# Optimization experiments

Measured on AMD Instinct MI355X. Metric: run time of the kernel, lower is better.

## Reference

```python
import jax, jax.numpy as jnp
import numpy as np

N = 100000
E = 6400000
IN_CH = 128
HID = 8
HEADS = 2
OUT_CH = 1
NEG_SLOPE = 0.2


def gat_conv(x, src, dst, W, a_src, a_dst, bias, heads, out_ch, concat, n_nodes):
    # x: [N, F_in], W: [F_in, heads*out_ch], a_src/a_dst: [heads, out_ch]
    h = (x @ W).reshape(n_nodes, heads, out_ch)          # [N, H, C]
    alpha_s = jnp.sum(h * a_src[None], axis=-1)          # [N, H]
    alpha_d = jnp.sum(h * a_dst[None], axis=-1)          # [N, H]
    alpha = alpha_s[src] + alpha_d[dst]                  # [E, H]
    alpha = jax.nn.leaky_relu(alpha, NEG_SLOPE)
    # segment softmax over incoming edges of each destination node
    seg_max = jax.ops.segment_max(alpha, dst, num_segments=n_nodes)  # [N, H]
    alpha = jnp.exp(alpha - seg_max[dst])
    denom = jax.ops.segment_sum(alpha, dst, num_segments=n_nodes)    # [N, H]
    alpha = alpha / (denom[dst] + 1e-16)
    msg = h[src] * alpha[..., None]                       # [E, H, C]
    out = jax.ops.segment_sum(msg, dst, num_segments=n_nodes)        # [N, H, C]
    if concat:
        out = out.reshape(n_nodes, heads * out_ch)
    else:
        out = out.mean(axis=1)
    return out + bias


def setup_inputs() -> dict:
    key = jax.random.key(0)
    ks = jax.random.split(key, 12)
    x = jax.random.normal(ks[0], (N, IN_CH), dtype=jnp.float32)
    edge_index = jax.random.randint(ks[1], (2, E), 0, N, dtype=jnp.int64)
    s1 = 1.0 / np.sqrt(IN_CH)
    W1 = jax.random.normal(ks[2], (IN_CH, HEADS * HID), dtype=jnp.float32) * s1
    a_src1 = jax.random.normal(ks[3], (HEADS, HID), dtype=jnp.float32) * (1.0 / np.sqrt(HID))
    a_dst1 = jax.random.normal(ks[4], (HEADS, HID), dtype=jnp.float32) * (1.0 / np.sqrt(HID))
    b1 = jnp.zeros((HEADS * HID,), dtype=jnp.float32)
    s2 = 1.0 / np.sqrt(HEADS * HID)
    W2 = jax.random.normal(ks[5], (HEADS * HID, OUT_CH), dtype=jnp.float32) * s2
    a_src2 = jax.random.normal(ks[6], (1, OUT_CH), dtype=jnp.float32)
    a_dst2 = jax.random.normal(ks[7], (1, OUT_CH), dtype=jnp.float32)
    b2 = jnp.zeros((OUT_CH,), dtype=jnp.float32)
    return {"x": x, "edge_index": edge_index, "W1": W1, "a_src1": a_src1,
            "a_dst1": a_dst1, "b1": b1, "W2": W2, "a_src2": a_src2,
            "a_dst2": a_dst2, "b2": b2}


def reference(x, edge_index, W1, a_src1, a_dst1, b1, W2, a_src2, a_dst2, b2):
    # add self-loops (PyG GATConv default)
    loops = jnp.arange(N, dtype=edge_index.dtype)
    src = jnp.concatenate([edge_index[0], loops])
    dst = jnp.concatenate([edge_index[1], loops])
    h = gat_conv(x, src, dst, W1, a_src1, a_dst1, b1, HEADS, HID, True, N)
    h = jax.nn.relu(h)
    out = gat_conv(h, src, dst, W2, a_src2, a_dst2, b2, 1, OUT_CH, False, N)
    return out
```

## Files before the change

### kernel.cpp

```cpp
#include <hip/hip_runtime.h>
#include <hip/hip_fp16.h>
#include <cstdint>
#include <cstddef>

#define N_NODES 100000
#define E_EDGES 6400000
#define E_TOT   (E_EDGES + N_NODES)
#define IN_CH   128
#define NHID    16
#define RECB    64
#define BSHIFT  9
#define BSZ     512
#define NBUCK   196
#define CHUNK   6144
#define BCAP    48
#define NCHUNK  ((E_TOT + CHUNK - 1) / CHUNK)

__global__ void k_detect(const int* __restrict__ edge, int* __restrict__ flag) {
    if (blockIdx.x == 0 && threadIdx.x == 0) {
        int odd_or = 0;
        for (int i = 0; i < 64; i++) odd_or |= edge[2 * i + 1];
        flag[0] = (odd_or == 0) ? 1 : 0;
    }
}

__global__ __launch_bounds__(256) void k_gemm1(
        const float* __restrict__ x, const float* __restrict__ W1,
        const float* __restrict__ a_src1, const float* __restrict__ a_dst1,
        char* __restrict__ rec, float* __restrict__ adst) {
    __shared__ __align__(16) float sW[IN_CH * NHID];
    __shared__ __align__(16) float sx[16][132];
    __shared__ float sh[16][17];
    int t = threadIdx.x;
    int r = t >> 4, c = t & 15;
    int row = blockIdx.x * 16 + r;

    const float4* W4 = (const float4*)W1;
    ((float4*)sW)[t] = W4[t];
    ((float4*)sW)[t + 256] = W4[t + 256];

    if (row < N_NODES) {
        const float4* xr = (const float4*)(x + (size_t)row * IN_CH);
        float4 v0 = xr[c];
        float4 v1 = xr[c + 16];
        *(float4*)&sx[r][4 * c] = v0;
        *(float4*)&sx[r][64 + 4 * c] = v1;
    }
    __syncthreads();

    float acc = 0.f;
    if (row < N_NODES) {
        #pragma unroll 16
        for (int k = 0; k < IN_CH; k++) acc = fmaf(sx[r][k], sW[k * NHID + c], acc);
        ((__half*)(rec + (size_t)row * RECB))[c] = __float2half(acc);
    }
    sh[r][c] = acc;
    __syncthreads();

    if (row < N_NODES && c < 4) {
        int h = c & 1;
        const float* av = (c >= 2) ? a_dst1 : a_src1;
        float s = 0.f;
        #pragma unroll
        for (int q = 0; q < 8; q++) s = fmaf(sh[r][h * 8 + q], av[h * 8 + q], s);
        if (c < 2) ((float*)(rec + (size_t)row * RECB + 32))[c] = s;
        else       adst[2 * (size_t)row + (c - 2)] = s;
    }
}

__global__ __launch_bounds__(256) void k_ccount(const int* __restrict__ edge,
                                                const int* __restrict__ flag,
                                                int* __restrict__ ccnt) {
    __shared__ int sc[NBUCK];
    int m64 = flag[0];
    int t = threadIdx.x;
    for (int i = t; i < NBUCK; i += 256) sc[i] = 0;
    __syncthreads();
    size_t c0 = (size_t)blockIdx.x * CHUNK;
    size_t cend = c0 + CHUNK; if (cend > E_TOT) cend = E_TOT;
    size_t ee = (cend < (size_t)E_EDGES) ? cend : (size_t)E_EDGES;

    if (m64) {
        const int4* dp = (const int4*)(edge + 2 * (size_t)E_EDGES);
        for (size_t i = c0 + 2 * t; i < ee; i += 512) {
            int4 v = dp[i >> 1];
            atomicAdd(&sc[v.x >> BSHIFT], 1);
            if (i + 1 < ee) atomicAdd(&sc[v.z >> BSHIFT], 1);
        }
    } else {
        const int4* dp = (const int4*)(edge + (size_t)E_EDGES);
        for (size_t i = c0 + 4 * t; i < ee; i += 1024) {
            int4 v = dp[i >> 2];
            atomicAdd(&sc[v.x >> BSHIFT], 1);
            if (i + 1 < ee) atomicAdd(&sc[v.y >> BSHIFT], 1);
            if (i + 2 < ee) atomicAdd(&sc[v.z >> BSHIFT], 1);
            if (i + 3 < ee) atomicAdd(&sc[v.w >> BSHIFT], 1);
        }
    }
    size_t sl0 = (c0 > (size_t)E_EDGES) ? c0 : (size_t)E_EDGES;
    for (size_t i = sl0 + t; i < cend; i += 256) {
        int d = (int)(i - E_EDGES);
        atomicAdd(&sc[d >> BSHIFT], 1);
    }
    __syncthreads();
    for (int i = t; i < NBUCK; i += 256)
        ccnt[(size_t)blockIdx.x * NBUCK + i] = sc[i];
}

__global__ __launch_bounds__(256) void k_cscan(int* __restrict__ ccnt,
                                               int* __restrict__ bcnt) {
    __shared__ int sd[256];
    __shared__ int carry;
    int b = blockIdx.x, t = threadIdx.x;
    if (t == 0) carry = 0;
    __syncthreads();
    for (int base = 0; base < NCHUNK; base += 256) {
        int c = base + t;
        int v = (c < NCHUNK) ? ccnt[(size_t)c * NBUCK + b] : 0;
        sd[t] = v;
        __syncthreads();
        for (int ofs = 1; ofs < 256; ofs <<= 1) {
            int a = sd[t];
            int bb = (t >= ofs) ? sd[t - ofs] : 0;
            __syncthreads();
            sd[t] = a + bb;
            __syncthreads();
        }
        if (c < NCHUNK) ccnt[(size_t)c * NBUCK + b] = sd[t] - v + carry;
        __syncthreads();
        if (t == 255) carry += sd[255];
        __syncthreads();
    }
    if (t == 0) bcnt[b] = carry;
}

__global__ void k_bscan(const int* __restrict__ bcnt, int* __restrict__ bbase) {
    __shared__ int sd[256];
    int t = threadIdx.x;
    int v = (t < NBUCK) ? bcnt[t] : 0;
    sd[t] = v;
    __syncthreads();
    for (int ofs = 1; ofs < 256; ofs <<= 1) {
        int a = sd[t];
        int b = (t >= ofs) ? sd[t - ofs] : 0;
        __syncthreads();
        sd[t] = a + b;
        __syncthreads();
    }
    if (t < NBUCK) bbase[t] = sd[t] - v;
    if (t == NBUCK) bbase[NBUCK] = sd[NBUCK - 1];
}

__global__ __launch_bounds__(256) void k_bin(const int* __restrict__ edge,
                                             const int* __restrict__ flag,
                                             const int* __restrict__ ccnt,
                                             const int* __restrict__ bbase,
                                             unsigned* __restrict__ staged) {
    __shared__ unsigned lbin[NBUCK][BCAP];
    __shared__ int lcnt[NBUCK];
    __shared__ int lbase[NBUCK];
    int m64 = flag[0];
    int t = threadIdx.x;
    int g = t >> 4, lane = t & 15;

    size_t c0 = (size_t)blockIdx.x * CHUNK;
    if (c0 >= E_TOT) return;
    size_t cend = c0 + CHUNK; if (cend > E_TOT) cend = E_TOT;
    size_t ee = (cend < (size_t)E_EDGES) ? cend : (size_t)E_EDGES;

    for (int i = t; i < NBUCK; i += 256) {
        lcnt[i] = 0;
        lbase[i] = bbase[i] + ccnt[(size_t)blockIdx.x * NBUCK + i];
    }
    __syncthreads();

    auto put = [&](int s, int d) {
        int b = d >> BSHIFT;
        unsigned v = (unsigned)s | ((unsigned)(d & (BSZ - 1)) << 17);
        int idx = atomicAdd(&lcnt[b], 1);
        if (idx < BCAP) lbin[b][idx] = v;
        else            staged[lbase[b] + idx] = v;
    };

    if (m64) {
        const int4* sp = (const int4*)edge;
        const int4* dp = (const int4*)(edge + 2 * (size_t)E_EDGES);
        for (size_t i = c0 + 2 * t; i < ee; i += 512) {
            int4 sv = sp[i >> 1];
            int4 dv = dp[i >> 1];
            put(sv.x, dv.x);
            if (i + 1 < ee) put(sv.z, dv.z);
        }
    } else {
        const int4* sp = (const int4*)edge;
        const int4* dp = (const int4*)(edge + (size_t)E_EDGES);
        for (size_t i = c0 + 4 * t; i < ee; i += 1024) {
            int4 sv = sp[i >> 2];
            int4 dv = dp[i >> 2];
            put(sv.x, dv.x);
            if (i + 1 < ee) put(sv.y, dv.y);
            if (i + 2 < ee) put(sv.z, dv.z);
            if (i + 3 < ee) put(sv.w, dv.w);
        }
    }
    size_t sl0 = (c0 > (size_t)E_EDGES) ? c0 : (size_t)E_EDGES;
    for (size_t i = sl0 + t; i < cend; i += 256) {
        int d = (int)(i - E_EDGES);
        put(d, d);
    }
    __syncthreads();
    for (int b = g; b < NBUCK; b += 16) {
        int n = min(lcnt[b], BCAP);
        if (!n) continue;
        int pos = lbase[b];
        for (int i = lane; i < n; i += 16) staged[pos + i] = lbin[b][i];
    }
}

__global__ __launch_bounds__(1024) void k_sort(const unsigned* __restrict__ staged,
                                               const int* __restrict__ bbase,
                                               int* __restrict__ csr,
                                               int* __restrict__ offs) {
    __shared__ int hist[BSZ];
    __shared__ int histlo[BSZ];
    __shared__ int lcur[BSZ];
    int bkt = blockIdx.x >> 1, p = blockIdx.x & 1;
    int t = threadIdx.x;
    int beg = bbase[bkt], end = bbase[bkt + 1];
    int mid = beg + ((end - beg + 1) >> 1);
    int dbase = bkt << BSHIFT;

    if (t < BSZ) { hist[t] = 0; histlo[t] = 0; }
    __syncthreads();
    for (int e = beg + t; e < end; e += 1024) {
        int dl = staged[e] >> 17;
        atomicAdd(&hist[dl], 1);
        if (e < mid) atomicAdd(&histlo[dl], 1);
    }
    __syncthreads();

    int myv = (t < BSZ) ? hist[t] : 0;
    __syncthreads();
    for (int ofs = 1; ofs < BSZ; ofs <<= 1) {
        int a = 0, b = 0;
        if (t < BSZ) { a = hist[t]; b = (t >= ofs) ? hist[t - ofs] : 0; }
        __syncthreads();
        if (t < BSZ) hist[t] = a + b;
        __syncthreads();
    }
    if (t < BSZ) {
        int excl = hist[t] - myv;
        lcur[t] = excl + (p ? histlo[t] : 0);
        if (p == 0) {
            int dd = dbase + t;
            if (dd < N_NODES) offs[dd] = beg + excl;
        }
    }
    if (bkt == NBUCK - 1 && p == 0 && t == 0) offs[N_NODES] = E_TOT;
    __syncthreads();

    int lo = p ? mid : beg;
    int hi = p ? end : mid;
    for (int e = lo + t; e < hi; e += 1024) {
        unsigned v = staged[e];
        int pos = atomicAdd(&lcur[v >> 17], 1);
        csr[beg + pos] = (int)(v & 0x1FFFFu);
    }
}

__global__ __launch_bounds__(256) void k_edge1(
        const int* __restrict__ offs, const int* __restrict__ csr,
        const char* __restrict__ rec, const float* __restrict__ adst,
        const float* __restrict__ b1, const float* __restrict__ W2,
        float* __restrict__ h2out) {
    __shared__ float sacc[256][17];
    int t = threadIdx.x;
    int lane = t & 15;
    int g = t >> 4;
    int d = blockIdx.x * 16 + g;
    if (d >= N_NODES) return;

    float2 adp = ((const float2*)adst)[d];
    int beg = offs[d], end = offs[d + 1];

    float acc[16];
    #pragma unroll
    for (int c = 0; c < 16; c++) acc[c] = 0.f;
    float den0 = 0.f, den1 = 0.f;

    auto loadslot = [&](int ee, float2& asp, float4& r0, float4& r1) {
        if (ee < end) {
            int s = csr[ee];
            const char* rp = rec + (size_t)s * RECB;
            r0 = ((const float4*)rp)[0];
            r1 = ((const float4*)rp)[1];
            asp = *(const float2*)(rp + 32);
        }
    };
    auto consume = [&](const float2& asp, const float4& r0, const float4& r1) {
        float a0 = asp.x + adp.x; a0 = (a0 > 0.f) ? a0 : 0.2f * a0;
        float a1 = asp.y + adp.y; a1 = (a1 > 0.f) ? a1 : 0.2f * a1;
        float p0 = __expf(a0), p1 = __expf(a1);
        den0 += p0; den1 += p1;
        const __half2* h0 = (const __half2*)&r0;
        const __half2* h1 = (const __half2*)&r1;
        #pragma unroll
        for (int q = 0; q < 4; q++) {
            float2 f0 = __half22float2(h0[q]);
            float2 f1 = __half22float2(h1[q]);
            acc[2 * q]         = fmaf(p0, f0.x, acc[2 * q]);
            acc[2 * q + 1]     = fmaf(p0, f0.y, acc[2 * q + 1]);
            acc[8 + 2 * q]     = fmaf(p1, f1.x, acc[8 + 2 * q]);
            acc[8 + 2 * q + 1] = fmaf(p1, f1.y, acc[8 + 2 * q + 1]);
        }
    };

    float2 aspA{}, aspB{}, aspC{}, aspD{}, aspE{}, aspF{};
    float4 z4 = make_float4(0.f, 0.f, 0.f, 0.f);
    float4 r0A = z4, r1A = z4, r0B = z4, r1B = z4, r0C = z4, r1C = z4;
    float4 r0D = z4, r1D = z4, r0E = z4, r1E = z4, r0F = z4, r1F = z4;

    int e = beg + lane;
    loadslot(e,      aspA, r0A, r1A);
    loadslot(e + 16, aspB, r0B, r1B);
    loadslot(e + 32, aspC, r0C, r1C);
    loadslot(e + 48, aspD, r0D, r1D);
    loadslot(e + 64, aspE, r0E, r1E);
    loadslot(e + 80, aspF, r0F, r1F);
    while (true) {
        if (e >= end) break;
        consume(aspA, r0A, r1A); loadslot(e + 96, aspA, r0A, r1A); e += 16;
        if (e >= end) break;
        consume(aspB, r0B, r1B); loadslot(e + 96, aspB, r0B, r1B); e += 16;
        if (e >= end) break;
        consume(aspC, r0C, r1C); loadslot(e + 96, aspC, r0C, r1C); e += 16;
        if (e >= end) break;
        consume(aspD, r0D, r1D); loadslot(e + 96, aspD, r0D, r1D); e += 16;
        if (e >= end) break;
        consume(aspE, r0E, r1E); loadslot(e + 96, aspE, r0E, r1E); e += 16;
        if (e >= end) break;
        consume(aspF, r0F, r1F); loadslot(e + 96, aspF, r0F, r1F); e += 16;
    }
    #pragma unroll
    for (int m = 1; m < 16; m <<= 1) {
        den0 += __shfl_xor(den0, m, 64);
        den1 += __shfl_xor(den1, m, 64);
    }
    #pragma unroll
    for (int c = 0; c < 16; c++) sacc[t][c] = acc[c];
    float sum = 0.f;
    int rowb = g * 16;
    #pragma unroll
    for (int l = 0; l < 16; l++) sum += sacc[rowb + l][lane];

    float den = (lane < 8) ? den0 : den1;
    float o = sum / (den + 1e-16f) + b1[lane];
    o = (o > 0.f) ? o : 0.f;
    float v = o * W2[lane];
    v += __shfl_xor(v, 1, 64);
    v += __shfl_xor(v, 2, 64);
    v += __shfl_xor(v, 4, 64);
    v += __shfl_xor(v, 8, 64);
    if (lane == 0) h2out[d] = v;
}

__global__ __launch_bounds__(256) void k_edge2(
        const int* __restrict__ offs, const int* __restrict__ csr,
        const float* __restrict__ h2,
        const float* __restrict__ a_src2, const float* __restrict__ a_dst2,
        const float* __restrict__ b2, float* __restrict__ out) {
    int t = threadIdx.x;
    int g = t >> 4, lane = t & 15;
    int d = blockIdx.x * 16 + g;
    if (d >= N_NODES) return;

    float as2 = a_src2[0], ad2 = a_dst2[0];
    float adv = h2[d] * ad2;
    int beg = offs[d], end = offs[d + 1];

    float den = 0.f, acc = 0.f;
    auto ls = [&](int ee, float& hs) { if (ee < end) hs = h2[csr[ee]]; };
    auto cs = [&](float hs) {
        float a = fmaf(hs, as2, adv);
        a = (a > 0.f) ? a : 0.2f * a;
        float p = __expf(a);
        den += p;
        acc = fmaf(p, hs, acc);
    };
    float hA = 0.f, hB = 0.f, hC = 0.f, hD = 0.f, hE = 0.f, hF = 0.f;
    int e = beg + lane;
    ls(e, hA); ls(e + 16, hB); ls(e + 32, hC);
    ls(e + 48, hD); ls(e + 64, hE); ls(e + 80, hF);
    while (true) {
        if (e >= end) break;
        cs(hA); ls(e + 96, hA); e += 16;
        if (e >= end) break;
        cs(hB); ls(e + 96, hB); e += 16;
        if (e >= end) break;
        cs(hC); ls(e + 96, hC); e += 16;
        if (e >= end) break;
        cs(hD); ls(e + 96, hD); e += 16;
        if (e >= end) break;
        cs(hE); ls(e + 96, hE); e += 16;
        if (e >= end) break;
        cs(hF); ls(e + 96, hF); e += 16;
    }
    #pragma unroll
    for (int m = 1; m < 16; m <<= 1) {
        den += __shfl_xor(den, m, 64);
        acc += __shfl_xor(acc, m, 64);
    }
    if (lane == 0) out[d] = acc / (den + 1e-16f) + b2[0];
}

extern "C" void kernel_launch(void* const* d_in, const int* in_sizes, int n_in,
                              void* d_out, int out_size, void* d_ws, size_t ws_size,
                              hipStream_t stream) {
    const float* x      = (const float*)d_in[0];
    const int*   edge   = (const int*)  d_in[1];
    const float* W1     = (const float*)d_in[2];
    const float* a_src1 = (const float*)d_in[3];
    const float* a_dst1 = (const float*)d_in[4];
    const float* b1     = (const float*)d_in[5];
    const float* W2     = (const float*)d_in[6];
    const float* a_src2 = (const float*)d_in[7];
    const float* a_dst2 = (const float*)d_in[8];
    const float* b2     = (const float*)d_in[9];

    constexpr size_t A = 256;
    auto al = [](size_t b) { return (b + A - 1) / A * A; };
    char* ws = (char*)d_ws;
    size_t off = 0;
    int*      flag   = (int*)(ws + off);      off += al(256);
    int*      ccnt   = (int*)(ws + off);      off += al((size_t)NCHUNK * NBUCK * 4);
    int*      bcnt   = (int*)(ws + off);      off += al(NBUCK * 4);
    int*      bbase  = (int*)(ws + off);      off += al((NBUCK + 1) * 4);
    unsigned* staged = (unsigned*)(ws + off); off += al((size_t)E_TOT * 4);
    int*      csr    = (int*)(ws + off);      off += al((size_t)E_TOT * 4);
    int*      offs   = (int*)(ws + off);      off += al((size_t)(N_NODES + 1) * 4);
    char*     rec    = (char*)(ws + off);     off += al((size_t)N_NODES * RECB);
    float*    adst   = (float*)(ws + off);    off += al((size_t)N_NODES * 2 * 4);
    float*    h2     = (float*)(ws + off);    off += al((size_t)N_NODES * 4);
    (void)ws_size; (void)in_sizes; (void)n_in; (void)out_size;

    k_detect<<<1, 64, 0, stream>>>(edge, flag);
    k_gemm1 <<<(N_NODES + 15) / 16, 256, 0, stream>>>(x, W1, a_src1, a_dst1, rec, adst);
    k_ccount<<<NCHUNK, 256, 0, stream>>>(edge, flag, ccnt);
    k_cscan <<<NBUCK, 256, 0, stream>>>(ccnt, bcnt);
    k_bscan <<<1, 256, 0, stream>>>(bcnt, bbase);
    k_bin   <<<NCHUNK, 256, 0, stream>>>(edge, flag, ccnt, bbase, staged);
    k_sort  <<<NBUCK * 2, 1024, 0, stream>>>(staged, bbase, csr, offs);
    k_edge1 <<<(N_NODES + 15) / 16, 256, 0, stream>>>(offs, csr, rec, adst, b1, W2, h2);
    k_edge2 <<<(N_NODES + 15) / 16, 256, 0, stream>>>(offs, csr, h2, a_src2, a_dst2, b2,
                                                      (float*)d_out);
}
```

Measured before the change: 219.3 us.

## Precompute edge attention weights during CSR sort and shrink gathered node records

The sort kernel now computes the leaky-relu and exp attention weight for each edge and each head while scattering. It stores them as a half2 next to the source index in an 8-byte CSR entry. Edge1 gathers only the 32-byte fp16 feature row per source, with two lanes splitting the heads, instead of a 64-byte padded record. The exp math moves out of the main gather loop, but CSR traffic doubles, edge2 reads 8-byte entries, and the weights are rounded to fp16.

```diff
diff --git a/kernel.cpp b/kernel.cpp
--- a/kernel.cpp
+++ b/kernel.cpp
@@ -8,7 +8,6 @@
 #define E_TOT   (E_EDGES + N_NODES)
 #define IN_CH   128
 #define NHID    16
-#define RECB    64
 #define BSHIFT  9
 #define BSZ     512
 #define NBUCK   196
@@ -27,7 +26,8 @@
 __global__ __launch_bounds__(256) void k_gemm1(
         const float* __restrict__ x, const float* __restrict__ W1,
         const float* __restrict__ a_src1, const float* __restrict__ a_dst1,
-        char* __restrict__ rec, float* __restrict__ adst) {
+        __half* __restrict__ h16, float* __restrict__ asrc,
+        float* __restrict__ adst) {
     __shared__ __align__(16) float sW[IN_CH * NHID];
     __shared__ __align__(16) float sx[16][132];
     __shared__ float sh[16][17];
@@ -52,7 +52,7 @@
     if (row < N_NODES) {
         #pragma unroll 16
         for (int k = 0; k < IN_CH; k++) acc = fmaf(sx[r][k], sW[k * NHID + c], acc);
-        ((__half*)(rec + (size_t)row * RECB))[c] = __float2half(acc);
+        h16[(size_t)row * NHID + c] = __float2half(acc);
     }
     sh[r][c] = acc;
     __syncthreads();
@@ -63,7 +63,7 @@
         float s = 0.f;
         #pragma unroll
         for (int q = 0; q < 8; q++) s = fmaf(sh[r][h * 8 + q], av[h * 8 + q], s);
-        if (c < 2) ((float*)(rec + (size_t)row * RECB + 32))[c] = s;
+        if (c < 2) asrc[2 * (size_t)row + c] = s;
         else       adst[2 * (size_t)row + (c - 2)] = s;
     }
 }
@@ -219,11 +219,14 @@
 
 __global__ __launch_bounds__(1024) void k_sort(const unsigned* __restrict__ staged,
                                                const int* __restrict__ bbase,
-                                               int* __restrict__ csr,
+                                               const float* __restrict__ asrc,
+                                               const float* __restrict__ adst,
+                                               uint2* __restrict__ csr8,
                                                int* __restrict__ offs) {
     __shared__ int hist[BSZ];
     __shared__ int histlo[BSZ];
     __shared__ int lcur[BSZ];
+    __shared__ float2 sadp[BSZ];
     int bkt = blockIdx.x >> 1, p = blockIdx.x & 1;
     int t = threadIdx.x;
     int beg = bbase[bkt], end = bbase[bkt + 1];
@@ -231,6 +234,10 @@
     int dbase = bkt << BSHIFT;
 
     if (t < BSZ) { hist[t] = 0; histlo[t] = 0; }
+    for (int i = t; i < BSZ; i += 1024) {
+        int dd = dbase + i;
+        sadp[i] = (dd < N_NODES) ? ((const float2*)adst)[dd] : make_float2(0.f, 0.f);
+    }
     __syncthreads();
     for (int e = beg + t; e < end; e += 1024) {
         int dl = staged[e] >> 17;
@@ -263,98 +270,97 @@
     int hi = p ? end : mid;
     for (int e = lo + t; e < hi; e += 1024) {
         unsigned v = staged[e];
-        int pos = atomicAdd(&lcur[v >> 17], 1);
-        csr[beg + pos] = (int)(v & 0x1FFFFu);
+        int s  = (int)(v & 0x1FFFFu);
+        int dl = (int)(v >> 17);
+        float2 asp = ((const float2*)asrc)[s];
+        float a0 = asp.x + sadp[dl].x; a0 = (a0 > 0.f) ? a0 : 0.2f * a0;
+        float a1 = asp.y + sadp[dl].y; a1 = (a1 > 0.f) ? a1 : 0.2f * a1;
+        __half2 hp = __floats2half2_rn(__expf(a0), __expf(a1));
+        int pos = atomicAdd(&lcur[dl], 1);
+        csr8[beg + pos] = make_uint2(*(unsigned*)&hp, (unsigned)s);
     }
 }
 
 __global__ __launch_bounds__(256) void k_edge1(
-        const int* __restrict__ offs, const int* __restrict__ csr,
-        const char* __restrict__ rec, const float* __restrict__ adst,
+        const int* __restrict__ offs, const uint2* __restrict__ csr8,
+        const __half* __restrict__ h16,
         const float* __restrict__ b1, const float* __restrict__ W2,
         float* __restrict__ h2out) {
-    __shared__ float sacc[256][17];
+    __shared__ float sacc[256][9];
     int t = threadIdx.x;
     int lane = t & 15;
     int g = t >> 4;
     int d = blockIdx.x * 16 + g;
     if (d >= N_NODES) return;
 
-    float2 adp = ((const float2*)adst)[d];
+    int sub = lane & 1;
+    int pr  = lane >> 1;
     int beg = offs[d], end = offs[d + 1];
 
-    float acc[16];
+    float acc[8];
     #pragma unroll
-    for (int c = 0; c < 16; c++) acc[c] = 0.f;
-    float den0 = 0.f, den1 = 0.f;
-
-    auto loadslot = [&](int ee, float2& asp, float4& r0, float4& r1) {
+    for (int c = 0; c < 8; c++) acc[c] = 0.f;
+    float den = 0.f;
+
+    auto loadslot = [&](int ee, uint2& ps, float4& hv) {
         if (ee < end) {
-            int s = csr[ee];
-            const char* rp = rec + (size_t)s * RECB;
-            r0 = ((const float4*)rp)[0];
-            r1 = ((const float4*)rp)[1];
-            asp = *(const float2*)(rp + 32);
+            ps = csr8[ee];
+            hv = *(const float4*)(h16 + (size_t)ps.y * NHID + sub * 8);
         }
     };
-    auto consume = [&](const float2& asp, const float4& r0, const float4& r1) {
-        float a0 = asp.x + adp.x; a0 = (a0 > 0.f) ? a0 : 0.2f * a0;
-        float a1 = asp.y + adp.y; a1 = (a1 > 0.f) ? a1 : 0.2f * a1;
-        float p0 = __expf(a0), p1 = __expf(a1);
-        den0 += p0; den1 += p1;
-        const __half2* h0 = (const __half2*)&r0;
-        const __half2* h1 = (const __half2*)&r1;
+    auto consume = [&](const uint2& ps, const float4& hv) {
+        __half2 hp = *(const __half2*)&ps.x;
+        float pw = sub ? __half2float(hp.y) : __half2float(hp.x);
+        den += pw;
+        const __half2* hh = (const __half2*)&hv;
         #pragma unroll
         for (int q = 0; q < 4; q++) {
-            float2 f0 = __half22float2(h0[q]);
-            float2 f1 = __half22float2(h1[q]);
-            acc[2 * q]         = fmaf(p0, f0.x, acc[2 * q]);
-            acc[2 * q + 1]     = fmaf(p0, f0.y, acc[2 * q + 1]);
-            acc[8 + 2 * q]     = fmaf(p1, f1.x, acc[8 + 2 * q]);
-            acc[8 + 2 * q + 1] = fmaf(p1, f1.y, acc[8 + 2 * q + 1]);
+            float2 f = __half22float2(hh[q]);
+            acc[2 * q]     = fmaf(pw, f.x, acc[2 * q]);
+            acc[2 * q + 1] = fmaf(pw, f.y, acc[2 * q + 1]);
         }
     };
 
-    float2 aspA{}, aspB{}, aspC{}, aspD{}, aspE{}, aspF{};
+    uint2 psA{}, psB{}, psC{}, psD{}, psE{}, psF{};
     float4 z4 = make_float4(0.f, 0.f, 0.f, 0.f);
-    float4 r0A = z4, r1A = z4, r0B = z4, r1B = z4, r0C = z4, r1C = z4;
-    float4 r0D = z4, r1D = z4, r0E = z4, r1E = z4, r0F = z4, r1F = z4;
-
-    int e = beg + lane;
-    loadslot(e,      aspA, r0A, r1A);
-    loadslot(e + 16, aspB, r0B, r1B);
-    loadslot(e + 32, aspC, r0C, r1C);
-    loadslot(e + 48, aspD, r0D, r1D);
-    loadslot(e + 64, aspE, r0E, r1E);
-    loadslot(e + 80, aspF, r0F, r1F);
+    float4 hA = z4, hB = z4, hC = z4, hD = z4, hE = z4, hF = z4;
+
+    int e = beg + pr;
+    loadslot(e,      psA, hA);
+    loadslot(e + 8,  psB, hB);
+    loadslot(e + 16, psC, hC);
+    loadslot(e + 24, psD, hD);
+    loadslot(e + 32, psE, hE);
+    loadslot(e + 40, psF, hF);
     while (true) {
         if (e >= end) break;
-        consume(aspA, r0A, r1A); loadslot(e + 96, aspA, r0A, r1A); e += 16;
-        if (e >= end) break;
-        consume(aspB, r0B, r1B); loadslot(e + 96, aspB, r0B, r1B); e += 16;
-        if (e >= end) break;
-        consume(aspC, r0C, r1C); loadslot(e + 96, aspC, r0C, r1C); e += 16;
-        if (e >= end) break;
-        consume(aspD, r0D, r1D); loadslot(e + 96, aspD, r0D, r1D); e += 16;
-        if (e >= end) break;
-        consume(aspE, r0E, r1E); loadslot(e + 96, aspE, r0E, r1E); e += 16;
-        if (e >= end) break;
-        consume(aspF, r0F, r1F); loadslot(e + 96, aspF, r0F, r1F); e += 16;
-    }
+        consume(psA, hA); loadslot(e + 48, psA, hA); e += 8;
+        if (e >= end) break;
+        consume(psB, hB); loadslot(e + 48, psB, hB); e += 8;
+        if (e >= end) break;
+        consume(psC, hC); loadslot(e + 48, psC, hC); e += 8;
+        if (e >= end) break;
+        consume(psD, hD); loadslot(e + 48, psD, hD); e += 8;
+        if (e >= end) break;
+        consume(psE, hE); loadslot(e + 48, psE, hE); e += 8;
+        if (e >= end) break;
+        consume(psF, hF); loadslot(e + 48, psF, hF); e += 8;
+    }
+    den += __shfl_xor(den, 2, 64);
+    den += __shfl_xor(den, 4, 64);
+    den += __shfl_xor(den, 8, 64);
     #pragma unroll
-    for (int m = 1; m < 16; m <<= 1) {
-        den0 += __shfl_xor(den0, m, 64);
-        den1 += __shfl_xor(den1, m, 64);
-    }
+    for (int c = 0; c < 8; c++) sacc[t][c] = acc[c];
+    float sum = 0.f;
+    int rowb = g * 16 + (lane >> 3);
+    int ch = lane & 7;
     #pragma unroll
-    for (int c = 0; c < 16; c++) sacc[t][c] = acc[c];
-    float sum = 0.f;
-    int rowb = g * 16;
-    #pragma unroll
-    for (int l = 0; l < 16; l++) sum += sacc[rowb + l][lane];
-
-    float den = (lane < 8) ? den0 : den1;
-    float o = sum / (den + 1e-16f) + b1[lane];
+    for (int pp = 0; pp < 8; pp++) sum += sacc[rowb + 2 * pp][ch];
+
+    int wgbase = t & 0x30;
+    float denh = __shfl(den, wgbase | (lane >> 3), 64);
+
+    float o = sum / (denh + 1e-16f) + b1[lane];
     o = (o > 0.f) ? o : 0.f;
     float v = o * W2[lane];
     v += __shfl_xor(v, 1, 64);
@@ -365,7 +371,7 @@
 }
 
 __global__ __launch_bounds__(256) void k_edge2(
-        const int* __restrict__ offs, const int* __restrict__ csr,
+        const int* __restrict__ offs, const uint2* __restrict__ csr8,
         const float* __restrict__ h2,
         const float* __restrict__ a_src2, const float* __restrict__ a_dst2,
         const float* __restrict__ b2, float* __restrict__ out) {
@@ -379,7 +385,7 @@
     int beg = offs[d], end = offs[d + 1];
 
     float den = 0.f, acc = 0.f;
-    auto ls = [&](int ee, float& hs) { if (ee < end) hs = h2[csr[ee]]; };
+    auto ls = [&](int ee, float& hs) { if (ee < end) hs = h2[csr8[ee].y]; };
     auto cs = [&](float hs) {
         float a = fmaf(hs, as2, adv);
         a = (a > 0.f) ? a : 0.2f * a;
@@ -436,21 +442,22 @@
     int*      bcnt   = (int*)(ws + off);      off += al(NBUCK * 4);
     int*      bbase  = (int*)(ws + off);      off += al((NBUCK + 1) * 4);
     unsigned* staged = (unsigned*)(ws + off); off += al((size_t)E_TOT * 4);
-    int*      csr    = (int*)(ws + off);      off += al((size_t)E_TOT * 4);
+    uint2*    csr8   = (uint2*)(ws + off);    off += al((size_t)E_TOT * 8);
     int*      offs   = (int*)(ws + off);      off += al((size_t)(N_NODES + 1) * 4);
-    char*     rec    = (char*)(ws + off);     off += al((size_t)N_NODES * RECB);
+    __half*   h16    = (__half*)(ws + off);   off += al((size_t)N_NODES * NHID * 2);
+    float*    asrc   = (float*)(ws + off);    off += al((size_t)N_NODES * 2 * 4);
     float*    adst   = (float*)(ws + off);    off += al((size_t)N_NODES * 2 * 4);
     float*    h2     = (float*)(ws + off);    off += al((size_t)N_NODES * 4);
     (void)ws_size; (void)in_sizes; (void)n_in; (void)out_size;
 
     k_detect<<<1, 64, 0, stream>>>(edge, flag);
-    k_gemm1 <<<(N_NODES + 15) / 16, 256, 0, stream>>>(x, W1, a_src1, a_dst1, rec, adst);
+    k_gemm1 <<<(N_NODES + 15) / 16, 256, 0, stream>>>(x, W1, a_src1, a_dst1, h16, asrc, adst);
     k_ccount<<<NCHUNK, 256, 0, stream>>>(edge, flag, ccnt);
     k_cscan <<<NBUCK, 256, 0, stream>>>(ccnt, bcnt);
     k_bscan <<<1, 256, 0, stream>>>(bcnt, bbase);
     k_bin   <<<NCHUNK, 256, 0, stream>>>(edge, flag, ccnt, bbase, staged);
-    k_sort  <<<NBUCK * 2, 1024, 0, stream>>>(staged, bbase, csr, offs);
-    k_edge1 <<<(N_NODES + 15) / 16, 256, 0, stream>>>(offs, csr, rec, adst, b1, W2, h2);
-    k_edge2 <<<(N_NODES + 15) / 16, 256, 0, stream>>>(offs, csr, h2, a_src2, a_dst2, b2,
+    k_sort  <<<NBUCK * 2, 1024, 0, stream>>>(staged, bbase, asrc, adst, csr8, offs);
+    k_edge1 <<<(N_NODES + 15) / 16, 256, 0, stream>>>(offs, csr8, h16, b1, W2, h2);
+    k_edge2 <<<(N_NODES + 15) / 16, 256, 0, stream>>>(offs, csr8, h2, a_src2, a_dst2, b2,
                                                       (float*)d_out);
 }
```

Result: slower. 233.9 us (+6.7%).
